# Kernel optimization log

Hardware: AMD Instinct MI355X
Metric: run time of the kernel (lower is better)

## Reference

```python
import jax, jax.numpy as jnp
import numpy as np

KH = KW = 5   # kernel_size
STRIDE = 1
PAD = 2


def _unfold(x, kh, kw, stride, pad):
    """Replicates F.unfold: returns (B, C*kh*kw, L) with channel slowest,
    then (i, j) within the kernel window (same ordering as torch)."""
    B, C, H, W = x.shape
    xp = jnp.pad(x, ((0, 0), (0, 0), (pad, pad), (pad, pad)))
    Ho = (H + 2 * pad - kh) // stride + 1
    Wo = (W + 2 * pad - kw) // stride + 1
    cols = []
    for i in range(kh):          # small fixed loop over kernel offsets (25 iters)
        for j in range(kw):
            cols.append(xp[:, :, i:i + stride * Ho:stride, j:j + stride * Wo:stride])
    # (B, C, kh*kw, Ho, Wo) -> (B, C*kh*kw, L)
    patches = jnp.stack(cols, axis=2)
    return patches.reshape(B, C * kh * kw, Ho * Wo), Ho, Wo


def setup_inputs() -> dict:
    key = jax.random.key(0)
    k1, k2 = jax.random.split(key)
    x = jax.random.normal(k1, (32, 3, 224, 224), dtype=jnp.float32)
    # kaiming_uniform-style init for weight (out_channels, in_ch*kh*kw)
    fan_in = 3 * KH * KW
    bound = np.sqrt(6.0 / fan_in)  # kaiming_uniform with a=sqrt(5) default gain approx
    weight = jax.random.uniform(k2, (64, fan_in), dtype=jnp.float32,
                                minval=-bound, maxval=bound)
    return {"x": x, "weight": weight}


def reference(x, weight):
    """RBF_Conv2d._cdist: euclidean distance between each receptive-field
    window and each prototype row of `weight`.
    x: (B, C, H, W), weight: (O, D=C*kh*kw) -> out: (B, O, Ho, Wo)."""
    B = x.shape[0]
    O = weight.shape[0]
    windows, Ho, Wo = _unfold(x, KH, KW, STRIDE, PAD)   # (B, D, L)
    windows = windows.transpose(0, 2, 1)                # (B, L, D)
    # cdist via ||p||^2 + ||w||^2 - 2 p.w (same trick torch.cdist uses)
    pn = jnp.sum(windows * windows, axis=-1)            # (B, L)
    wn = jnp.sum(weight * weight, axis=-1)              # (O,)
    dots = jnp.einsum('bld,od->blo', windows, weight)   # (B, L, O)
    d2 = pn[:, :, None] + wn[None, None, :] - 2.0 * dots
    dist = jnp.sqrt(jnp.maximum(d2, 0.0))               # (B, L, O)
    return dist.transpose(0, 2, 1).reshape(B, O, Ho, Wo)
```

## Files before the change

kernel.cpp:

```cpp
#include <hip/hip_runtime.h>
#include <hip/hip_bf16.h>
#include <math.h>


#define KH 5
#define KW 5
#define PAD 2
#define CH 3
#define DD 75
#define OC 64
#define HH 224
#define WW 224
#define HW (HH * WW)
#define NSX 7
#define RPB 7

using short8_t = __attribute__((ext_vector_type(8))) short;
using f32x16   = __attribute__((ext_vector_type(16))) float;

union Oct { unsigned int w[4]; short8_t v; };

__device__ inline unsigned int rne_bf16(float v) {
    return (unsigned int)__builtin_bit_cast(unsigned short, __float2bfloat16(v));
}

__device__ inline float fsqrt_fast(float x) {
    float r;
    asm("v_sqrt_f32 %0, %1" : "=v"(r) : "v"(x));
    return r;
}

template<bool EDGE>
__device__ inline float xelem(const float* __restrict__ xb, int y, int xp, int d) {
    if (d >= DD) return 0.f;
    const int c = d / 25, rem = d % 25, i = rem / 5, j = rem % 5;
    int gy = y + i - PAD;
    int gx = xp + j;
    if constexpr (!EDGE) {
        return xb[(c * HH + gy) * WW + gx];
    } else {
        bool ok = ((unsigned)gy < (unsigned)HH) & ((unsigned)gx < (unsigned)WW);
        int gyc = min(max(gy, 0), HH - 1);
        int gxc = min(max(gx, 0), WW - 1);
        float raw = xb[(c * HH + gyc) * WW + gxc];
        return ok ? raw : 0.f;
    }
}

template<int D0, bool EDGE>
__device__ inline void build_oct_rne(const float* __restrict__ xb, int y, int xp,
                                     float& pn, Oct& b) {
#pragma unroll
    for (int rr = 0; rr < 8; rr += 2) {
        float v0 = xelem<EDGE>(xb, y, xp, D0 + rr);
        float v1 = xelem<EDGE>(xb, y, xp, D0 + rr + 1);
        pn = fmaf(v0, v0, pn);
        pn = fmaf(v1, v1, pn);
        b.w[rr >> 1] = rne_bf16(v0) | (rne_bf16(v1) << 16);
    }
}

template<int D0>
__device__ inline void build_aoct_wn(const float* wrow, Oct& a, float& wns) {
#pragma unroll
    for (int rr = 0; rr < 8; rr += 2) {
        float r0 = (D0 + rr     < DD) ? wrow[D0 + rr]     : 0.f;
        float r1 = (D0 + rr + 1 < DD) ? wrow[D0 + rr + 1] : 0.f;
        wns = fmaf(r0, r0, wns);
        wns = fmaf(r1, r1, wns);
        a.w[rr >> 1] = rne_bf16(-2.f * r0) | (rne_bf16(-2.f * r1) << 16);
    }
}

#define MFMA(A, B, C) __builtin_amdgcn_mfma_f32_32x32x16_bf16((A), (B), (C), 0, 0, 0)

template<bool EDGE>
__device__ inline void do_strip(const float* __restrict__ xb, int y, int xp, int hi,
                                const Oct (&ah)[2][5], float* __restrict__ op) {
    float pnp = 0.f;
    Oct bh[5];
    if (hi == 0) {
        build_oct_rne<0,  EDGE>(xb, y, xp, pnp, bh[0]);
        build_oct_rne<16, EDGE>(xb, y, xp, pnp, bh[1]);
        build_oct_rne<32, EDGE>(xb, y, xp, pnp, bh[2]);
        build_oct_rne<48, EDGE>(xb, y, xp, pnp, bh[3]);
        build_oct_rne<64, EDGE>(xb, y, xp, pnp, bh[4]);
    } else {
        build_oct_rne<8,  EDGE>(xb, y, xp, pnp, bh[0]);
        build_oct_rne<24, EDGE>(xb, y, xp, pnp, bh[1]);
        build_oct_rne<40, EDGE>(xb, y, xp, pnp, bh[2]);
        build_oct_rne<56, EDGE>(xb, y, xp, pnp, bh[3]);
        build_oct_rne<72, EDGE>(xb, y, xp, pnp, bh[4]);
    }
    float pn = pnp + __shfl_xor(pnp, 32);
    if (hi == 1) {
        unsigned int up  = __builtin_bit_cast(unsigned int, pn);
        float pnhv = __builtin_bit_cast(float, up & 0xFFFF0000u);
        unsigned int pnl = rne_bf16(pn - pnhv);
        bh[4].w[1] |= 0x3F800000u;
        bh[4].w[2]  = 0x3F80u | (up & 0xFFFF0000u);
        bh[4].w[3]  = pnl;
    }

    f32x16 acc0 = {0.f,0.f,0.f,0.f,0.f,0.f,0.f,0.f,0.f,0.f,0.f,0.f,0.f,0.f,0.f,0.f};
    f32x16 acc1 = acc0;
#pragma unroll
    for (int st = 0; st < 5; ++st) {
        acc0 = MFMA(ah[0][st].v, bh[st].v, acc0);
        acc1 = MFMA(ah[1][st].v, bh[st].v, acc1);
    }

#pragma unroll
    for (int reg = 0; reg < 16; ++reg) {
        int ob = (reg & 3) + 8 * (reg >> 2);
        op[(size_t)ob * HW]        = fsqrt_fast(fmaxf(acc0[reg], 0.f));
        op[(size_t)(ob + 32) * HW] = fsqrt_fast(fmaxf(acc1[reg], 0.f));
    }
}

__global__ __launch_bounds__(256, 4) void rbf_mfma(const float* __restrict__ x,
                                                   const float* __restrict__ w,
                                                   float* __restrict__ out) {
    __shared__ float wlds[OC * DD];
    const int tid  = threadIdx.x;

    for (int idx = tid; idx < OC * DD; idx += 256)
        wlds[idx] = w[idx];
    __syncthreads();

    const int lane = tid & 63;
    const int l31  = lane & 31;
    const int hi   = lane >> 5;

    float wnp[2] = {0.f, 0.f};
    Oct ah[2][5];
    if (hi == 0) {
#pragma unroll
        for (int mt = 0; mt < 2; ++mt) {
            const float* wrow = wlds + (l31 + 32 * mt) * DD;
            build_aoct_wn<0 >(wrow, ah[mt][0], wnp[mt]);
            build_aoct_wn<16>(wrow, ah[mt][1], wnp[mt]);
            build_aoct_wn<32>(wrow, ah[mt][2], wnp[mt]);
            build_aoct_wn<48>(wrow, ah[mt][3], wnp[mt]);
            build_aoct_wn<64>(wrow, ah[mt][4], wnp[mt]);
        }
    } else {
#pragma unroll
        for (int mt = 0; mt < 2; ++mt) {
            const float* wrow = wlds + (l31 + 32 * mt) * DD;
            build_aoct_wn<8 >(wrow, ah[mt][0], wnp[mt]);
            build_aoct_wn<24>(wrow, ah[mt][1], wnp[mt]);
            build_aoct_wn<40>(wrow, ah[mt][2], wnp[mt]);
            build_aoct_wn<56>(wrow, ah[mt][3], wnp[mt]);
            build_aoct_wn<72>(wrow, ah[mt][4], wnp[mt]);
        }
    }
    float wn0 = wnp[0] + __shfl_xor(wnp[0], 32);
    float wn1 = wnp[1] + __shfl_xor(wnp[1], 32);
    if (hi == 1) {
#pragma unroll
        for (int mt = 0; mt < 2; ++mt) {
            float wnv = mt ? wn1 : wn0;
            unsigned int uwn = __builtin_bit_cast(unsigned int, wnv);
            float wnhv = __builtin_bit_cast(float, uwn & 0xFFFF0000u);
            unsigned int wnl = rne_bf16(wnv - wnhv);
            ah[mt][4].w[1] = (ah[mt][4].w[1] & 0xFFFFu) | (uwn & 0xFFFF0000u);
            ah[mt][4].w[2] = wnl | (0x3F80u << 16);
            ah[mt][4].w[3] = 0x3F80u;
        }
    }

    const int b  = blockIdx.x >> 5;
    const int y0 = (blockIdx.x & 31) * RPB;
    const int wv = tid >> 6;
    const float* xb = x + (size_t)b * (CH * HW);
    float* outb = out + (size_t)b * OC * HW + (size_t)hi * 4 * HW + l31;

    const int niter = (wv == 0) ? 13 : 12;
#pragma unroll 1
    for (int it = 0; it < niter; ++it) {
        int sidx = it * 4 + wv;
        int r    = (sidx * 37) >> 8;
        int sx   = sidx - r * 7;
        int y    = y0 + r;
        int x0   = sx * 32;
        int xp   = x0 + l31 - PAD;
        float* op = outb + (size_t)y * WW + x0;
        bool interior = (y >= PAD) & (y < HH - PAD) & (sx >= 1) & (sx <= 5);
        if (interior) do_strip<false>(xb, y, xp, hi, ah, op);
        else          do_strip<true >(xb, y, xp, hi, ah, op);
    }
}

extern "C" void kernel_launch(void* const* d_in, const int* in_sizes, int n_in,
                              void* d_out, int out_size, void* d_ws, size_t ws_size,
                              hipStream_t stream) {
    const float* x = (const float*)d_in[0];
    const float* w = (const float*)d_in[1];
    float* out     = (float*)d_out;

    int B       = in_sizes[0] / (CH * HW);
    int nblocks = B * 32;

    rbf_mfma<<<nblocks, 256, 0, stream>>>(x, w, out);
}
```

Baseline: 113.4 us.

## Stage MFMA outputs in LDS and write rows with 128-bit coalesced stores

Each per-lane scalar store of the 64-channel result is replaced by a write into an LDS tile of 64 channels by 128 columns. The block then stores it to global memory as contiguous float4 rows per output channel. Each image row is processed in two phases of 128 and 96 columns, separated by block-wide barriers. This should improve store coalescing and vector width, at the cost of extra barriers, idle waves in the second phase (only 3 of 4 compute), and less overlap between compute and stores.

```diff
diff --git a/kernel.cpp b/kernel.cpp
--- a/kernel.cpp
+++ b/kernel.cpp
@@ -12,11 +12,12 @@
 #define HH 224
 #define WW 224
 #define HW (HH * WW)
-#define NSX 7
 #define RPB 7
+#define TW 128
 
 using short8_t = __attribute__((ext_vector_type(8))) short;
 using f32x16   = __attribute__((ext_vector_type(16))) float;
+using f32x4    = __attribute__((ext_vector_type(4))) float;
 
 union Oct { unsigned int w[4]; short8_t v; };
 
@@ -76,7 +77,7 @@
 
 template<bool EDGE>
 __device__ inline void do_strip(const float* __restrict__ xb, int y, int xp, int hi,
-                                const Oct (&ah)[2][5], float* __restrict__ op) {
+                                const Oct (&ah)[2][5], float* lds, int ctile) {
     float pnp = 0.f;
     Oct bh[5];
     if (hi == 0) {
@@ -112,20 +113,20 @@
 
 #pragma unroll
     for (int reg = 0; reg < 16; ++reg) {
-        int ob = (reg & 3) + 8 * (reg >> 2);
-        op[(size_t)ob * HW]        = fsqrt_fast(fmaxf(acc0[reg], 0.f));
-        op[(size_t)(ob + 32) * HW] = fsqrt_fast(fmaxf(acc1[reg], 0.f));
+        int ob = (reg & 3) + 8 * (reg >> 2) + 4 * hi;
+        lds[ob * TW + ctile]        = fsqrt_fast(fmaxf(acc0[reg], 0.f));
+        lds[(ob + 32) * TW + ctile] = fsqrt_fast(fmaxf(acc1[reg], 0.f));
     }
 }
 
 __global__ __launch_bounds__(256, 4) void rbf_mfma(const float* __restrict__ x,
                                                    const float* __restrict__ w,
                                                    float* __restrict__ out) {
-    __shared__ float wlds[OC * DD];
+    __shared__ float lds[OC * TW];
     const int tid  = threadIdx.x;
 
     for (int idx = tid; idx < OC * DD; idx += 256)
-        wlds[idx] = w[idx];
+        lds[idx] = w[idx];
     __syncthreads();
 
     const int lane = tid & 63;
@@ -137,7 +138,7 @@
     if (hi == 0) {
 #pragma unroll
         for (int mt = 0; mt < 2; ++mt) {
-            const float* wrow = wlds + (l31 + 32 * mt) * DD;
+            const float* wrow = lds + (l31 + 32 * mt) * DD;
             build_aoct_wn<0 >(wrow, ah[mt][0], wnp[mt]);
             build_aoct_wn<16>(wrow, ah[mt][1], wnp[mt]);
             build_aoct_wn<32>(wrow, ah[mt][2], wnp[mt]);
@@ -147,7 +148,7 @@
     } else {
 #pragma unroll
         for (int mt = 0; mt < 2; ++mt) {
-            const float* wrow = wlds + (l31 + 32 * mt) * DD;
+            const float* wrow = lds + (l31 + 32 * mt) * DD;
             build_aoct_wn<8 >(wrow, ah[mt][0], wnp[mt]);
             build_aoct_wn<24>(wrow, ah[mt][1], wnp[mt]);
             build_aoct_wn<40>(wrow, ah[mt][2], wnp[mt]);
@@ -169,26 +170,59 @@
             ah[mt][4].w[3] = 0x3F80u;
         }
     }
+    __syncthreads();
 
     const int b  = blockIdx.x >> 5;
     const int y0 = (blockIdx.x & 31) * RPB;
     const int wv = tid >> 6;
     const float* xb = x + (size_t)b * (CH * HW);
-    float* outb = out + (size_t)b * OC * HW + (size_t)hi * 4 * HW + l31;
-
-    const int niter = (wv == 0) ? 13 : 12;
+    float* outb = out + (size_t)b * OC * HW;
+
+    const int wp   = tid >> 5;
+    const int slot = tid & 31;
+
 #pragma unroll 1
-    for (int it = 0; it < niter; ++it) {
-        int sidx = it * 4 + wv;
-        int r    = (sidx * 37) >> 8;
-        int sx   = sidx - r * 7;
-        int y    = y0 + r;
-        int x0   = sx * 32;
-        int xp   = x0 + l31 - PAD;
-        float* op = outb + (size_t)y * WW + x0;
-        bool interior = (y >= PAD) & (y < HH - PAD) & (sx >= 1) & (sx <= 5);
-        if (interior) do_strip<false>(xb, y, xp, hi, ah, op);
-        else          do_strip<true >(xb, y, xp, hi, ah, op);
+    for (int r = 0; r < RPB; ++r) {
+        int y = r + y0;
+        bool yin = (y >= PAD) & (y < HH - PAD);
+
+        {
+            int sx = wv;
+            int xp = sx * 32 + l31 - PAD;
+            int ct = sx * 32 + l31;
+            if (yin & (sx >= 1)) do_strip<false>(xb, y, xp, hi, ah, lds, ct);
+            else                 do_strip<true >(xb, y, xp, hi, ah, lds, ct);
+        }
+        __syncthreads();
+        {
+            float* orow = outb + (size_t)y * WW + slot * 4;
+#pragma unroll
+            for (int it = 0; it < 8; ++it) {
+                int o = it * 8 + wp;
+                f32x4 v = *(const f32x4*)&lds[o * TW + slot * 4];
+                *(f32x4*)(orow + (size_t)o * HW) = v;
+            }
+        }
+        __syncthreads();
+
+        if (wv < 3) {
+            int sx = 4 + wv;
+            int xp = sx * 32 + l31 - PAD;
+            int ct = (sx - 4) * 32 + l31;
+            if (yin & (sx <= 5)) do_strip<false>(xb, y, xp, hi, ah, lds, ct);
+            else                 do_strip<true >(xb, y, xp, hi, ah, lds, ct);
+        }
+        __syncthreads();
+        if (slot < 24) {
+            float* orow = outb + (size_t)y * WW + 128 + slot * 4;
+#pragma unroll
+            for (int it = 0; it < 8; ++it) {
+                int o = it * 8 + wp;
+                f32x4 v = *(const f32x4*)&lds[o * TW + slot * 4];
+                *(f32x4*)(orow + (size_t)o * HW) = v;
+            }
+        }
+        __syncthreads();
     }
 }
 
```

Result: slower. 220.4 us (+94.4%).

## Split output channels across wave pairs to halve registers and raise occupancy

Applied to the files above, without the earlier changes.

Each wave now computes only one 32-channel half of the outputs, so it holds one set of weight fragments and one accumulator instead of two. Wave pairs share a strip, and the block covers 4 rows instead of 7, giving more blocks and a launch-bounds target of 5 blocks per CU. This lowers register pressure and should improve latency hiding. The cost is that each strip's input patches are gathered and converted twice, once per channel half, which doubles input loads and bf16 conversion work.

```diff
diff --git a/kernel.cpp b/kernel.cpp
--- a/kernel.cpp
+++ b/kernel.cpp
@@ -13,7 +13,7 @@
 #define WW 224
 #define HW (HH * WW)
 #define NSX 7
-#define RPB 7
+#define RPB 4
 
 using short8_t = __attribute__((ext_vector_type(8))) short;
 using f32x16   = __attribute__((ext_vector_type(16))) float;
@@ -76,7 +76,7 @@
 
 template<bool EDGE>
 __device__ inline void do_strip(const float* __restrict__ xb, int y, int xp, int hi,
-                                const Oct (&ah)[2][5], float* __restrict__ op) {
+                                const Oct (&ah)[5], float* __restrict__ op) {
     float pnp = 0.f;
     Oct bh[5];
     if (hi == 0) {
@@ -102,23 +102,19 @@
         bh[4].w[3]  = pnl;
     }
 
-    f32x16 acc0 = {0.f,0.f,0.f,0.f,0.f,0.f,0.f,0.f,0.f,0.f,0.f,0.f,0.f,0.f,0.f,0.f};
-    f32x16 acc1 = acc0;
+    f32x16 acc = {0.f,0.f,0.f,0.f,0.f,0.f,0.f,0.f,0.f,0.f,0.f,0.f,0.f,0.f,0.f,0.f};
 #pragma unroll
-    for (int st = 0; st < 5; ++st) {
-        acc0 = MFMA(ah[0][st].v, bh[st].v, acc0);
-        acc1 = MFMA(ah[1][st].v, bh[st].v, acc1);
-    }
+    for (int st = 0; st < 5; ++st)
+        acc = MFMA(ah[st].v, bh[st].v, acc);
 
 #pragma unroll
     for (int reg = 0; reg < 16; ++reg) {
         int ob = (reg & 3) + 8 * (reg >> 2);
-        op[(size_t)ob * HW]        = fsqrt_fast(fmaxf(acc0[reg], 0.f));
-        op[(size_t)(ob + 32) * HW] = fsqrt_fast(fmaxf(acc1[reg], 0.f));
+        op[(size_t)ob * HW] = fsqrt_fast(fmaxf(acc[reg], 0.f));
     }
 }
 
-__global__ __launch_bounds__(256, 4) void rbf_mfma(const float* __restrict__ x,
+__global__ __launch_bounds__(256, 5) void rbf_mfma(const float* __restrict__ x,
                                                    const float* __restrict__ w,
                                                    float* __restrict__ out) {
     __shared__ float wlds[OC * DD];
@@ -128,64 +124,56 @@
         wlds[idx] = w[idx];
     __syncthreads();
 
-    const int lane = tid & 63;
-    const int l31  = lane & 31;
-    const int hi   = lane >> 5;
+    const int lane  = tid & 63;
+    const int l31   = lane & 31;
+    const int hi    = lane >> 5;
+    const int wv    = tid >> 6;
+    const int ohalf = wv & 1;
+    const int sp    = wv >> 1;
 
-    float wnp[2] = {0.f, 0.f};
-    Oct ah[2][5];
+    float wnp = 0.f;
+    Oct ah[5];
+    const float* wrow = wlds + (l31 + 32 * ohalf) * DD;
     if (hi == 0) {
-#pragma unroll
-        for (int mt = 0; mt < 2; ++mt) {
-            const float* wrow = wlds + (l31 + 32 * mt) * DD;
-            build_aoct_wn<0 >(wrow, ah[mt][0], wnp[mt]);
-            build_aoct_wn<16>(wrow, ah[mt][1], wnp[mt]);
-            build_aoct_wn<32>(wrow, ah[mt][2], wnp[mt]);
-            build_aoct_wn<48>(wrow, ah[mt][3], wnp[mt]);
-            build_aoct_wn<64>(wrow, ah[mt][4], wnp[mt]);
-        }
+        build_aoct_wn<0 >(wrow, ah[0], wnp);
+        build_aoct_wn<16>(wrow, ah[1], wnp);
+        build_aoct_wn<32>(wrow, ah[2], wnp);
+        build_aoct_wn<48>(wrow, ah[3], wnp);
+        build_aoct_wn<64>(wrow, ah[4], wnp);
     } else {
-#pragma unroll
-        for (int mt = 0; mt < 2; ++mt) {
-            const float* wrow = wlds + (l31 + 32 * mt) * DD;
-            build_aoct_wn<8 >(wrow, ah[mt][0], wnp[mt]);
-            build_aoct_wn<24>(wrow, ah[mt][1], wnp[mt]);
-            build_aoct_wn<40>(wrow, ah[mt][2], wnp[mt]);
-            build_aoct_wn<56>(wrow, ah[mt][3], wnp[mt]);
-            build_aoct_wn<72>(wrow, ah[mt][4], wnp[mt]);
-        }
+        build_aoct_wn<8 >(wrow, ah[0], wnp);
+        build_aoct_wn<24>(wrow, ah[1], wnp);
+        build_aoct_wn<40>(wrow, ah[2], wnp);
+        build_aoct_wn<56>(wrow, ah[3], wnp);
+        build_aoct_wn<72>(wrow, ah[4], wnp);
     }
-    float wn0 = wnp[0] + __shfl_xor(wnp[0], 32);
-    float wn1 = wnp[1] + __shfl_xor(wnp[1], 32);
+    float wn = wnp + __shfl_xor(wnp, 32);
     if (hi == 1) {
-#pragma unroll
-        for (int mt = 0; mt < 2; ++mt) {
-            float wnv = mt ? wn1 : wn0;
-            unsigned int uwn = __builtin_bit_cast(unsigned int, wnv);
-            float wnhv = __builtin_bit_cast(float, uwn & 0xFFFF0000u);
-            unsigned int wnl = rne_bf16(wnv - wnhv);
-            ah[mt][4].w[1] = (ah[mt][4].w[1] & 0xFFFFu) | (uwn & 0xFFFF0000u);
-            ah[mt][4].w[2] = wnl | (0x3F80u << 16);
-            ah[mt][4].w[3] = 0x3F80u;
-        }
+        unsigned int uwn = __builtin_bit_cast(unsigned int, wn);
+        float wnhv = __builtin_bit_cast(float, uwn & 0xFFFF0000u);
+        unsigned int wnl = rne_bf16(wn - wnhv);
+        ah[4].w[1] = (ah[4].w[1] & 0xFFFFu) | (uwn & 0xFFFF0000u);
+        ah[4].w[2] = wnl | (0x3F80u << 16);
+        ah[4].w[3] = 0x3F80u;
     }
 
-    const int b  = blockIdx.x >> 5;
-    const int y0 = (blockIdx.x & 31) * RPB;
-    const int wv = tid >> 6;
+    const int bi    = blockIdx.x;
+    const int b     = bi / 56;
+    const int chunk = bi - b * 56;
+    const int y0    = chunk * RPB;
     const float* xb = x + (size_t)b * (CH * HW);
-    float* outb = out + (size_t)b * OC * HW + (size_t)hi * 4 * HW + l31;
+    float* outw = out + (size_t)b * OC * HW
+                      + (size_t)(ohalf * 32 + hi * 4) * HW + l31;
 
-    const int niter = (wv == 0) ? 13 : 12;
 #pragma unroll 1
-    for (int it = 0; it < niter; ++it) {
-        int sidx = it * 4 + wv;
+    for (int it = 0; it < 2 * NSX; ++it) {
+        int sidx = it * 2 + sp;
         int r    = (sidx * 37) >> 8;
         int sx   = sidx - r * 7;
         int y    = y0 + r;
         int x0   = sx * 32;
         int xp   = x0 + l31 - PAD;
-        float* op = outb + (size_t)y * WW + x0;
+        float* op = outw + (size_t)y * WW + x0;
         bool interior = (y >= PAD) & (y < HH - PAD) & (sx >= 1) & (sx <= 5);
         if (interior) do_strip<false>(xb, y, xp, hi, ah, op);
         else          do_strip<true >(xb, y, xp, hi, ah, op);
@@ -200,7 +188,7 @@
     float* out     = (float*)d_out;
 
     int B       = in_sizes[0] / (CH * HW);
-    int nblocks = B * 32;
+    int nblocks = B * 56;
 
     rbf_mfma<<<nblocks, 256, 0, stream>>>(x, w, out);
 }
```

Result: slower. 140.8 us (+24.2%).

## Interleave B-operand construction with MFMAs and shrink rows per block

Applied to the files above, without the earlier changes.

The strip routine now builds one bf16 B-fragment at a time and issues its two MFMAs immediately, instead of materialising all five fragments before the matrix loop. This cuts live registers so launch bounds can request 5 blocks per SIMD, and it lets loads and conversions overlap with MFMA execution. The grid is repartitioned from 7 rows per block (32 blocks per image) to 5 rows (45 chunks, the last one partial), which gives more, smaller blocks for better occupancy and load balance. The cost is more per-block weight staging and fragment setup, plus a ragged final chunk.

```diff
diff --git a/kernel.cpp b/kernel.cpp
--- a/kernel.cpp
+++ b/kernel.cpp
@@ -13,7 +13,8 @@
 #define WW 224
 #define HW (HH * WW)
 #define NSX 7
-#define RPB 7
+#define RPB 5
+#define CPI 45
 
 using short8_t = __attribute__((ext_vector_type(8))) short;
 using f32x16   = __attribute__((ext_vector_type(16))) float;
@@ -77,38 +78,39 @@
 template<bool EDGE>
 __device__ inline void do_strip(const float* __restrict__ xb, int y, int xp, int hi,
                                 const Oct (&ah)[2][5], float* __restrict__ op) {
+    f32x16 acc0 = {0.f,0.f,0.f,0.f,0.f,0.f,0.f,0.f,0.f,0.f,0.f,0.f,0.f,0.f,0.f,0.f};
+    f32x16 acc1 = acc0;
     float pnp = 0.f;
-    Oct bh[5];
-    if (hi == 0) {
-        build_oct_rne<0,  EDGE>(xb, y, xp, pnp, bh[0]);
-        build_oct_rne<16, EDGE>(xb, y, xp, pnp, bh[1]);
-        build_oct_rne<32, EDGE>(xb, y, xp, pnp, bh[2]);
-        build_oct_rne<48, EDGE>(xb, y, xp, pnp, bh[3]);
-        build_oct_rne<64, EDGE>(xb, y, xp, pnp, bh[4]);
-    } else {
-        build_oct_rne<8,  EDGE>(xb, y, xp, pnp, bh[0]);
-        build_oct_rne<24, EDGE>(xb, y, xp, pnp, bh[1]);
-        build_oct_rne<40, EDGE>(xb, y, xp, pnp, bh[2]);
-        build_oct_rne<56, EDGE>(xb, y, xp, pnp, bh[3]);
-        build_oct_rne<72, EDGE>(xb, y, xp, pnp, bh[4]);
-    }
+    Oct b;
+
+    if (hi == 0) build_oct_rne<0,  EDGE>(xb, y, xp, pnp, b);
+    else         build_oct_rne<8,  EDGE>(xb, y, xp, pnp, b);
+    acc0 = MFMA(ah[0][0].v, b.v, acc0); acc1 = MFMA(ah[1][0].v, b.v, acc1);
+
+    if (hi == 0) build_oct_rne<16, EDGE>(xb, y, xp, pnp, b);
+    else         build_oct_rne<24, EDGE>(xb, y, xp, pnp, b);
+    acc0 = MFMA(ah[0][1].v, b.v, acc0); acc1 = MFMA(ah[1][1].v, b.v, acc1);
+
+    if (hi == 0) build_oct_rne<32, EDGE>(xb, y, xp, pnp, b);
+    else         build_oct_rne<40, EDGE>(xb, y, xp, pnp, b);
+    acc0 = MFMA(ah[0][2].v, b.v, acc0); acc1 = MFMA(ah[1][2].v, b.v, acc1);
+
+    if (hi == 0) build_oct_rne<48, EDGE>(xb, y, xp, pnp, b);
+    else         build_oct_rne<56, EDGE>(xb, y, xp, pnp, b);
+    acc0 = MFMA(ah[0][3].v, b.v, acc0); acc1 = MFMA(ah[1][3].v, b.v, acc1);
+
+    if (hi == 0) build_oct_rne<64, EDGE>(xb, y, xp, pnp, b);
+    else         build_oct_rne<72, EDGE>(xb, y, xp, pnp, b);
     float pn = pnp + __shfl_xor(pnp, 32);
     if (hi == 1) {
         unsigned int up  = __builtin_bit_cast(unsigned int, pn);
         float pnhv = __builtin_bit_cast(float, up & 0xFFFF0000u);
         unsigned int pnl = rne_bf16(pn - pnhv);
-        bh[4].w[1] |= 0x3F800000u;
-        bh[4].w[2]  = 0x3F80u | (up & 0xFFFF0000u);
-        bh[4].w[3]  = pnl;
-    }
-
-    f32x16 acc0 = {0.f,0.f,0.f,0.f,0.f,0.f,0.f,0.f,0.f,0.f,0.f,0.f,0.f,0.f,0.f,0.f};
-    f32x16 acc1 = acc0;
-#pragma unroll
-    for (int st = 0; st < 5; ++st) {
-        acc0 = MFMA(ah[0][st].v, bh[st].v, acc0);
-        acc1 = MFMA(ah[1][st].v, bh[st].v, acc1);
-    }
+        b.w[1] |= 0x3F800000u;
+        b.w[2]  = 0x3F80u | (up & 0xFFFF0000u);
+        b.w[3]  = pnl;
+    }
+    acc0 = MFMA(ah[0][4].v, b.v, acc0); acc1 = MFMA(ah[1][4].v, b.v, acc1);
 
 #pragma unroll
     for (int reg = 0; reg < 16; ++reg) {
@@ -118,7 +120,7 @@
     }
 }
 
-__global__ __launch_bounds__(256, 4) void rbf_mfma(const float* __restrict__ x,
+__global__ __launch_bounds__(256, 5) void rbf_mfma(const float* __restrict__ x,
                                                    const float* __restrict__ w,
                                                    float* __restrict__ out) {
     __shared__ float wlds[OC * DD];
@@ -170,13 +172,17 @@
         }
     }
 
-    const int b  = blockIdx.x >> 5;
-    const int y0 = (blockIdx.x & 31) * RPB;
-    const int wv = tid >> 6;
+    const int bi    = blockIdx.x;
+    const int b     = bi / CPI;
+    const int chunk = bi - b * CPI;
+    const int y0    = chunk * RPB;
+    const int nrows = min(RPB, HH - y0);
+    const int nstr  = nrows * NSX;
+    const int wv    = tid >> 6;
     const float* xb = x + (size_t)b * (CH * HW);
     float* outb = out + (size_t)b * OC * HW + (size_t)hi * 4 * HW + l31;
 
-    const int niter = (wv == 0) ? 13 : 12;
+    const int niter = (nstr - wv + 3) >> 2;
 #pragma unroll 1
     for (int it = 0; it < niter; ++it) {
         int sidx = it * 4 + wv;
@@ -200,7 +206,7 @@
     float* out     = (float*)d_out;
 
     int B       = in_sizes[0] / (CH * HW);
-    int nblocks = B * 32;
+    int nblocks = B * CPI;
 
     rbf_mfma<<<nblocks, 256, 0, stream>>>(x, w, out);
 }
```

Result: slower. 229.3 us (+102.2%).
